# Optimization experiments

Hardware: AMD Instinct MI355X
Metric: run time of the kernel (lower is better)

Reference implementation:

```python
import jax, jax.numpy as jnp
import numpy as np

HEADS, DEPTH, KS = 4, 16, 3
PAD = KS // 2
LN_EPS = 1e-3   # keras LayerNormalization default
BN_EPS = 1e-3   # keras BatchNormalization default


def _layernorm(x, g, b):
    m = jnp.mean(x, axis=-1, keepdims=True)
    v = jnp.var(x, axis=-1, keepdims=True)
    return (x - m) * jax.lax.rsqrt(v + LN_EPS) * g + b


def setup_inputs() -> dict:
    key = jax.random.key(0)
    ks = jax.random.split(key, 12)
    B, H, W, C, FF = 4, 384, 384, 64, 128
    s = 0.05
    return {
        "x": jax.random.normal(ks[0], (B, H, W, C), jnp.float32),
        "wq": jax.random.normal(ks[1], (C, C), jnp.float32) * s,
        "wk": jax.random.normal(ks[2], (C, C), jnp.float32) * s,
        "wv": jax.random.normal(ks[3], (C, C), jnp.float32) * s,
        "ln1_g": jnp.ones((C,), jnp.float32),
        "ln1_b": jnp.zeros((C,), jnp.float32),
        "ff1_w": jax.random.normal(ks[4], (C, FF), jnp.float32) * s,
        "ff1_b": jnp.zeros((FF,), jnp.float32),
        "ff2_w": jax.random.normal(ks[5], (FF, C), jnp.float32) * s,
        "ff2_b": jnp.zeros((C,), jnp.float32),
        "ln2_g": jnp.ones((C,), jnp.float32),
        "ln2_b": jnp.zeros((C,), jnp.float32),
        "w_fuse": jax.random.normal(ks[6], (C, C), jnp.float32) * s,
        "bn_g": jax.random.uniform(ks[7], (C,), jnp.float32, 0.5, 1.5),
        "bn_b": jax.random.normal(ks[8], (C,), jnp.float32) * s,
        "bn_mean": jax.random.normal(ks[9], (C,), jnp.float32) * s,
        "bn_var": jax.random.uniform(ks[10], (C,), jnp.float32, 0.5, 1.5),
    }


def reference(x, wq, wk, wv, ln1_g, ln1_b, ff1_w, ff1_b, ff2_w, ff2_b,
              ln2_g, ln2_b, w_fuse, bn_g, bn_b, bn_mean, bn_var):
    B, H, W, C = x.shape
    # 1x1-conv projections == per-pixel dense over channels
    q = jnp.einsum('bhwc,cd->bhwd', x, wq).reshape(B, H, W, HEADS, DEPTH)
    k = jnp.einsum('bhwc,cd->bhwd', x, wk)
    v = jnp.einsum('bhwc,cd->bhwd', x, wv)
    # SAME zero-padding, matching tf.image.extract_patches
    kp = jnp.pad(k, ((0, 0), (PAD, PAD), (PAD, PAD), (0, 0)))
    vp = jnp.pad(v, ((0, 0), (PAD, PAD), (PAD, PAD), (0, 0)))
    # scores for each of the ks*ks offsets via shifted slices (no im2col blowup)
    sims = []
    for dy in range(KS):
        for dx in range(KS):
            ksh = kp[:, dy:dy + H, dx:dx + W, :].reshape(B, H, W, HEADS, DEPTH)
            sims.append(jnp.einsum('bhwnd,bhwnd->bhwn', q, ksh))
    sim = jnp.stack(sims, axis=3) / jnp.sqrt(jnp.float32(DEPTH))  # [B,H,W,ka,heads]
    attn = jax.nn.softmax(sim, axis=3)
    out = jnp.zeros_like(q)  # [B,H,W,heads,depth]
    i = 0
    for dy in range(KS):
        for dx in range(KS):
            vsh = vp[:, dy:dy + H, dx:dx + W, :].reshape(B, H, W, HEADS, DEPTH)
            out = out + attn[:, :, :, i, :, None] * vsh
            i += 1
    out = out.reshape(B, H, W, C)
    # residual (res_proj is None since C % heads == 0) + LN
    out = _layernorm(x + out, ln1_g, ln1_b)
    # token FFN with residual + LN
    ff = jax.nn.relu(jnp.einsum('bhwc,cf->bhwf', out, ff1_w) + ff1_b)
    ff = jnp.einsum('bhwf,fc->bhwc', ff, ff2_w) + ff2_b
    out = _layernorm(out + ff, ln2_g, ln2_b)
    # fuse 1x1 conv + BN (inference mode, moving stats) + relu
    out = jnp.einsum('bhwc,cd->bhwd', out, w_fuse)
    scale = bn_g * jax.lax.rsqrt(bn_var + BN_EPS)
    out = out * scale + (bn_b - bn_mean * scale)
    return jax.nn.relu(out)
```

## Files before the change

kernel.cpp:

```cpp
#include <hip/hip_runtime.h>

#define MTOT 589824

typedef __attribute__((ext_vector_type(8))) short bf16x8;
typedef __attribute__((ext_vector_type(4))) float f32x4;
#define MFMA16 __builtin_amdgcn_mfma_f32_16x16x32_bf16

__device__ __forceinline__ unsigned short f2bf(float f) {
    union { float f; unsigned u; } x; x.f = f;
    unsigned r = x.u + 0x7FFFu + ((x.u >> 16) & 1u);
    return (unsigned short)(r >> 16);
}
__device__ __forceinline__ float bf2f(unsigned short h) {
    union { unsigned u; float f; } x; x.u = ((unsigned)h) << 16;
    return x.f;
}
__device__ __forceinline__ float2 bfpair(int v) {
    union { unsigned u; float f; } a, b;
    a.u = ((unsigned)v) << 16;
    b.u = ((unsigned)v) & 0xffff0000u;
    return make_float2(a.f, b.f);
}
__device__ __forceinline__ int is_bf16(const void* ln1g) {
    return ((const unsigned short*)ln1g)[0] != 0;
}
__device__ __forceinline__ float ldp(const void* p, int i, int isbf) {
    return isbf ? bf2f(((const unsigned short*)p)[i]) : ((const float*)p)[i];
}

__global__ void k_prep(const void* wq, const void* wk, const void* wv,
                       const void* ln1g, const void* ln1b,
                       const void* ff1w, const void* ff1b,
                       const void* ff2w, const void* ff2b,
                       const void* ln2g, const void* ln2b,
                       const void* wfuse, const void* bng, const void* bnb,
                       const void* bnm, const void* bnv,
                       unsigned short* Wbase, float* P) {
    const int isbf = is_bf16(ln1g);
    const int tid = blockIdx.x * blockDim.x + threadIdx.x;
    const int stride = gridDim.x * blockDim.x;
    unsigned short* Wqkv = Wbase;
    unsigned short* W1 = Wbase + 12288;
    unsigned short* W2 = W1 + 8192;
    unsigned short* WF = W2 + 8192;
    for (int i = tid; i < 12288; i += stride) {
        int n = i >> 6, k = i & 63;
        float v;
        if (n < 64)        v = ldp(wq, k*64 + n, isbf) * 0.25f;
        else if (n < 128)  v = ldp(wk, k*64 + (n-64), isbf);
        else               v = ldp(wv, k*64 + (n-128), isbf);
        Wqkv[n*64 + k] = f2bf(v);
    }
    for (int i = tid; i < 8192; i += stride) {
        int n = i >> 6, k = i & 63;
        W1[n*64 + k] = f2bf(ldp(ff1w, k*128 + n, isbf));
    }
    for (int i = tid; i < 8192; i += stride) {
        int n = i >> 7, k = i & 127;
        W2[n*128 + k] = f2bf(ldp(ff2w, k*64 + n, isbf));
    }
    for (int i = tid; i < 4096; i += stride) {
        int n = i >> 6, k = i & 63;
        WF[n*64 + k] = f2bf(ldp(wfuse, k*64 + n, isbf));
    }
    for (int i = tid; i < 64; i += stride) {
        P[i]       = ldp(ln1g, i, isbf);
        P[64+i]    = ldp(ln1b, i, isbf);
        P[256+i]   = ldp(ff2b, i, isbf);
        P[320+i]   = ldp(ln2g, i, isbf);
        P[384+i]   = ldp(ln2b, i, isbf);
        float sc   = ldp(bng, i, isbf) * rsqrtf(ldp(bnv, i, isbf) + 1e-3f);
        P[448+i]   = sc;
        P[512+i]   = ldp(bnb, i, isbf) - ldp(bnm, i, isbf) * sc;
    }
    for (int i = tid; i < 128; i += stride) P[128+i] = ldp(ff1b, i, isbf);
}

__global__ __launch_bounds__(256) void k_qkv(const void* __restrict__ xg,
                                             const void* __restrict__ ln1g,
                                             const unsigned short* __restrict__ Wqkv,
                                             unsigned short* __restrict__ qp,
                                             unsigned short* __restrict__ kvp) {
    __shared__ unsigned short lA[64*72];
    __shared__ unsigned short stg[64*200];
    const int t = threadIdx.x;
    const long m0 = (long)blockIdx.x * 64;
    if (is_bf16(ln1g)) {
        const unsigned short* xs = (const unsigned short*)xg + m0*64;
        #pragma unroll
        for (int j = 0; j < 2; ++j) {
            int e = (j*256 + t)*8, r = e >> 6, c = e & 63;
            *(int4*)&lA[r*72 + c] = *(const int4*)(xs + e);
        }
    } else {
        const float* xs = (const float*)xg + m0*64;
        #pragma unroll
        for (int j = 0; j < 4; ++j) {
            int e = (j*256 + t)*4, r = e >> 6, c = e & 63;
            float4 f = *(const float4*)(xs + e);
            ushort4 h;
            h.x = f2bf(f.x); h.y = f2bf(f.y); h.z = f2bf(f.z); h.w = f2bf(f.w);
            *(ushort4*)&lA[r*72 + c] = h;
        }
    }
    __syncthreads();
    const int w = t >> 6, l = t & 63, lm = l & 15, q4 = l >> 4;
    const bf16x8 a0 = *(const bf16x8*)&lA[(w*16 + lm)*72 + q4*8];
    const bf16x8 a1 = *(const bf16x8*)&lA[(w*16 + lm)*72 + 32 + q4*8];
    #pragma unroll
    for (int nt = 0; nt < 12; ++nt) {
        const unsigned short* wp = Wqkv + (nt*16 + lm)*64 + q4*8;
        bf16x8 b0 = *(const bf16x8*)wp;
        bf16x8 b1 = *(const bf16x8*)(wp + 32);
        f32x4 acc = {0.f, 0.f, 0.f, 0.f};
        acc = MFMA16(a0, b0, acc, 0, 0, 0);
        acc = MFMA16(a1, b1, acc, 0, 0, 0);
        #pragma unroll
        for (int r = 0; r < 4; ++r)
            stg[(w*16 + q4*4 + r)*200 + nt*16 + lm] = f2bf(acc[r]);
    }
    __syncthreads();
    const size_t P16 = (size_t)MTOT * 16, P32 = (size_t)MTOT * 32;
    #pragma unroll
    for (int j = 0; j < 2; ++j) {
        int idx = j*256 + t;
        int h = idx >> 7, rem = idx & 127, px = rem >> 1, part = rem & 1;
        *(int4*)(qp + (size_t)h*P16 + (m0 + px)*16 + part*8) =
            *(const int4*)&stg[px*200 + h*16 + part*8];
    }
    #pragma unroll
    for (int j = 0; j < 4; ++j) {
        int idx = j*256 + t;
        int h = idx >> 8, rem = idx & 255, px = rem >> 2, part = rem & 3;
        int scol = (part < 2) ? (64 + h*16 + part*8) : (128 + h*16 + (part-2)*8);
        *(int4*)(kvp + (size_t)h*P32 + (m0 + px)*32 + part*8) =
            *(const int4*)&stg[px*200 + scol];
    }
}

__global__ __launch_bounds__(256) void k_attn(unsigned short* __restrict__ qp,
                                              const unsigned short* __restrict__ kvp) {
    __shared__ unsigned short kvh[324*36];
    const int t = threadIdx.x;
    const int h = blockIdx.x & 3;
    const int tile = blockIdx.x >> 2;
    const int bx = tile % 24;
    const int by = (tile / 24) % 24;
    const int bb = tile / 576;
    const long imgbase = (long)bb * 384 * 384;
    const unsigned short* kvplane = kvp + (size_t)h * MTOT * 32;
    unsigned short* qplane = qp + (size_t)h * MTOT * 16;

    for (int i = t; i < 2592; i += 256) {
        int p = i >> 3, part = i & 7;
        int hy = p / 18, hx = p - hy*18;
        int gy = by*16 + hy - 1, gx = bx*16 + hx - 1;
        int2 val = {0, 0};
        if (gy >= 0 && gy < 384 && gx >= 0 && gx < 384)
            val = *(const int2*)(kvplane + (imgbase + (long)gy*384 + gx)*32 + part*4);
        *(int2*)&kvh[p*36 + part*4] = val;
    }
    __syncthreads();

    const int tx = t & 15, ty = t >> 4;
    const long pix = imgbase + (long)(by*16 + ty)*384 + bx*16 + tx;
    float qv[16];
    {
        const int4 qa = *(const int4*)(qplane + pix*16);
        const int4 qb = *(const int4*)(qplane + pix*16 + 8);
        float2 p0;
        p0 = bfpair(qa.x); qv[0]  = p0.x; qv[1]  = p0.y;
        p0 = bfpair(qa.y); qv[2]  = p0.x; qv[3]  = p0.y;
        p0 = bfpair(qa.z); qv[4]  = p0.x; qv[5]  = p0.y;
        p0 = bfpair(qa.w); qv[6]  = p0.x; qv[7]  = p0.y;
        p0 = bfpair(qb.x); qv[8]  = p0.x; qv[9]  = p0.y;
        p0 = bfpair(qb.y); qv[10] = p0.x; qv[11] = p0.y;
        p0 = bfpair(qb.z); qv[12] = p0.x; qv[13] = p0.y;
        p0 = bfpair(qb.w); qv[14] = p0.x; qv[15] = p0.y;
    }
    float w9[9];
    #pragma unroll
    for (int e = 0; e < 9; ++e) {
        int dy = e / 3, dx = e - dy*3;
        const int2* kp = (const int2*)&kvh[((ty+dy)*18 + tx+dx)*36];
        float sacc = 0.f;
        #pragma unroll
        for (int j = 0; j < 4; ++j) {
            int2 kk = kp[j];
            float2 pa = bfpair(kk.x), pb = bfpair(kk.y);
            sacc += qv[j*4+0]*pa.x + qv[j*4+1]*pa.y
                  + qv[j*4+2]*pb.x + qv[j*4+3]*pb.y;
        }
        w9[e] = sacc;
    }
    float mx = w9[0];
    #pragma unroll
    for (int e = 1; e < 9; ++e) mx = fmaxf(mx, w9[e]);
    float den = 0.f;
    #pragma unroll
    for (int e = 0; e < 9; ++e) { w9[e] = __expf(w9[e] - mx); den += w9[e]; }
    const float inv = 1.f / den;
    float att[16];
    #pragma unroll
    for (int i = 0; i < 16; ++i) att[i] = 0.f;
    #pragma unroll
    for (int e = 0; e < 9; ++e) {
        int dy = e / 3, dx = e - dy*3;
        const int2* vp = (const int2*)&kvh[((ty+dy)*18 + tx+dx)*36 + 16];
        const float wgt = w9[e] * inv;
        #pragma unroll
        for (int j = 0; j < 4; ++j) {
            int2 vv = vp[j];
            float2 pa = bfpair(vv.x), pb = bfpair(vv.y);
            att[j*4+0] += wgt*pa.x;
            att[j*4+1] += wgt*pa.y;
            att[j*4+2] += wgt*pb.x;
            att[j*4+3] += wgt*pb.y;
        }
    }
    int4 o0, o1;
    o0.x = (int)((unsigned)f2bf(att[0])  | ((unsigned)f2bf(att[1])  << 16));
    o0.y = (int)((unsigned)f2bf(att[2])  | ((unsigned)f2bf(att[3])  << 16));
    o0.z = (int)((unsigned)f2bf(att[4])  | ((unsigned)f2bf(att[5])  << 16));
    o0.w = (int)((unsigned)f2bf(att[6])  | ((unsigned)f2bf(att[7])  << 16));
    o1.x = (int)((unsigned)f2bf(att[8])  | ((unsigned)f2bf(att[9])  << 16));
    o1.y = (int)((unsigned)f2bf(att[10]) | ((unsigned)f2bf(att[11]) << 16));
    o1.z = (int)((unsigned)f2bf(att[12]) | ((unsigned)f2bf(att[13]) << 16));
    o1.w = (int)((unsigned)f2bf(att[14]) | ((unsigned)f2bf(att[15]) << 16));
    *(int4*)(qplane + pix*16)     = o0;
    *(int4*)(qplane + pix*16 + 8) = o1;
}

__global__ __launch_bounds__(256) void k_tail(const unsigned short* __restrict__ attp,
                                              const void* __restrict__ xg,
                                              const void* __restrict__ ln1g,
                                              const unsigned short* __restrict__ W1,
                                              const unsigned short* __restrict__ W2,
                                              const unsigned short* __restrict__ WF,
                                              const float* __restrict__ P,
                                              void* __restrict__ outg) {
    __shared__ unsigned short lA[64*72];
    __shared__ unsigned short hbuf[64*136];
    const int t = threadIdx.x;
    const long m0 = (long)blockIdx.x * 64;
    const int isbf = is_bf16(ln1g);
    const size_t P16 = (size_t)MTOT * 16;
    #pragma unroll
    for (int j = 0; j < 2; ++j) {
        int idx = j*256 + t;
        int h = idx >> 7, rem = idx & 127, px = rem >> 1, part = rem & 1;
        *(int4*)&lA[px*72 + h*16 + part*8] =
            *(const int4*)(attp + (size_t)h*P16 + (m0 + px)*16 + part*8);
    }
    __syncthreads();
    {
        const int px = t >> 2, qtr = t & 3;
        float v[16];
        const int2* ap = (const int2*)&lA[px*72 + qtr*16];
        #pragma unroll
        for (int j = 0; j < 4; ++j) {
            int2 u = ap[j];
            float2 pa = bfpair(u.x), pb = bfpair(u.y);
            v[j*4+0] = pa.x; v[j*4+1] = pa.y; v[j*4+2] = pb.x; v[j*4+3] = pb.y;
        }
        if (isbf) {
            const int4* xp = (const int4*)((const unsigned short*)xg + (m0 + px)*64 + qtr*16);
            #pragma unroll
            for (int j = 0; j < 2; ++j) {
                int4 u = xp[j];
                float2 pa = bfpair(u.x), pb = bfpair(u.y), pc = bfpair(u.z), pd = bfpair(u.w);
                v[j*8+0] += pa.x; v[j*8+1] += pa.y;
                v[j*8+2] += pb.x; v[j*8+3] += pb.y;
                v[j*8+4] += pc.x; v[j*8+5] += pc.y;
                v[j*8+6] += pd.x; v[j*8+7] += pd.y;
            }
        } else {
            const float4* xp = (const float4*)((const float*)xg + (m0 + px)*64 + qtr*16);
            #pragma unroll
            for (int j = 0; j < 4; ++j) {
                float4 f = xp[j];
                v[j*4+0] += f.x; v[j*4+1] += f.y; v[j*4+2] += f.z; v[j*4+3] += f.w;
            }
        }
        float s = 0.f, ss = 0.f;
        #pragma unroll
        for (int c = 0; c < 16; ++c) { s += v[c]; ss += v[c]*v[c]; }
        s  += __shfl_xor(s, 1);  ss += __shfl_xor(ss, 1);
        s  += __shfl_xor(s, 2);  ss += __shfl_xor(ss, 2);
        const float mean = s * (1.f/64.f);
        const float var  = ss * (1.f/64.f) - mean*mean;
        const float rs   = rsqrtf(var + 1e-3f);
        unsigned short* wp = &lA[px*72 + qtr*16];
        #pragma unroll
        for (int c = 0; c < 16; ++c)
            wp[c] = f2bf((v[c] - mean)*rs*P[qtr*16 + c] + P[64 + qtr*16 + c]);
    }
    __syncthreads();
    const int w = t >> 6, l = t & 63, lm = l & 15, q4 = l >> 4;
    {
        const bf16x8 a0 = *(const bf16x8*)&lA[(w*16 + lm)*72 + q4*8];
        const bf16x8 a1 = *(const bf16x8*)&lA[(w*16 + lm)*72 + 32 + q4*8];
        #pragma unroll
        for (int nt = 0; nt < 8; ++nt) {
            const unsigned short* wp = W1 + (nt*16 + lm)*64 + q4*8;
            bf16x8 b0 = *(const bf16x8*)wp;
            bf16x8 b1 = *(const bf16x8*)(wp + 32);
            f32x4 acc = {0.f, 0.f, 0.f, 0.f};
            acc = MFMA16(a0, b0, acc, 0, 0, 0);
            acc = MFMA16(a1, b1, acc, 0, 0, 0);
            const float bias = P[128 + nt*16 + lm];
            #pragma unroll
            for (int r = 0; r < 4; ++r)
                hbuf[(w*16 + q4*4 + r)*136 + nt*16 + lm] = f2bf(fmaxf(acc[r] + bias, 0.f));
        }
    }
    __syncthreads();
    {
        bf16x8 a[4];
        #pragma unroll
        for (int kc = 0; kc < 4; ++kc)
            a[kc] = *(const bf16x8*)&hbuf[(w*16 + lm)*136 + kc*32 + q4*8];
        float v[4][4];
        #pragma unroll
        for (int nt = 0; nt < 4; ++nt) {
            f32x4 acc = {0.f, 0.f, 0.f, 0.f};
            #pragma unroll
            for (int kc = 0; kc < 4; ++kc) {
                bf16x8 b = *(const bf16x8*)(W2 + (nt*16 + lm)*128 + kc*32 + q4*8);
                acc = MFMA16(a[kc], b, acc, 0, 0, 0);
            }
            const int col = nt*16 + lm;
            const float bias = P[256 + col];
            #pragma unroll
            for (int r = 0; r < 4; ++r)
                v[nt][r] = acc[r] + bias + bf2f(lA[(w*16 + q4*4 + r)*72 + col]);
        }
        float s[4], ss[4];
        #pragma unroll
        for (int r = 0; r < 4; ++r) {
            s[r]  = v[0][r] + v[1][r] + v[2][r] + v[3][r];
            ss[r] = v[0][r]*v[0][r] + v[1][r]*v[1][r] + v[2][r]*v[2][r] + v[3][r]*v[3][r];
        }
        #pragma unroll
        for (int mk = 1; mk <= 8; mk <<= 1) {
            #pragma unroll
            for (int r = 0; r < 4; ++r) {
                s[r]  += __shfl_xor(s[r], mk);
                ss[r] += __shfl_xor(ss[r], mk);
            }
        }
        __syncthreads();
        #pragma unroll
        for (int r = 0; r < 4; ++r) {
            const float mean = s[r] * (1.f/64.f);
            const float var  = ss[r] * (1.f/64.f) - mean*mean;
            const float rsv  = rsqrtf(var + 1e-3f);
            #pragma unroll
            for (int nt = 0; nt < 4; ++nt) {
                const int col = nt*16 + lm;
                lA[(w*16 + q4*4 + r)*72 + col] =
                    f2bf((v[nt][r] - mean)*rsv*P[320 + col] + P[384 + col]);
            }
        }
    }
    __syncthreads();
    {
        const bf16x8 a0 = *(const bf16x8*)&lA[(w*16 + lm)*72 + q4*8];
        const bf16x8 a1 = *(const bf16x8*)&lA[(w*16 + lm)*72 + 32 + q4*8];
        float* stf = (float*)hbuf + w*1024;
        unsigned short* sth = hbuf + w*1024;
        #pragma unroll
        for (int nt = 0; nt < 4; ++nt) {
            const unsigned short* wp = WF + (nt*16 + lm)*64 + q4*8;
            bf16x8 b0 = *(const bf16x8*)wp;
            bf16x8 b1 = *(const bf16x8*)(wp + 32);
            f32x4 acc = {0.f, 0.f, 0.f, 0.f};
            acc = MFMA16(a0, b0, acc, 0, 0, 0);
            acc = MFMA16(a1, b1, acc, 0, 0, 0);
            const int col = nt*16 + lm;
            const float sc = P[448 + col], bi = P[512 + col];
            #pragma unroll
            for (int r = 0; r < 4; ++r) {
                float f = fmaxf(acc[r]*sc + bi, 0.f);
                if (isbf) sth[(q4*4 + r)*64 + col] = f2bf(f);
                else      stf[(q4*4 + r)*64 + col] = f;
            }
        }
    }
    __syncthreads();
    if (isbf) {
        const unsigned short* sth = hbuf + w*1024;
        unsigned short* orow = (unsigned short*)outg + m0*64;
        #pragma unroll
        for (int i = 0; i < 2; ++i) {
            int e = (i*64 + l)*8, r = e >> 6, c = e & 63;
            *(int4*)(orow + (long)(w*16 + r)*64 + c) = *(const int4*)&sth[e];
        }
    } else {
        const float* stf = (const float*)hbuf + w*1024;
        float* orow = (float*)outg + m0*64;
        #pragma unroll
        for (int i = 0; i < 4; ++i) {
            int e = (i*64 + l)*4, r = e >> 6, c = e & 63;
            *(float4*)(orow + (long)(w*16 + r)*64 + c) = *(const float4*)&stf[e];
        }
    }
}

extern "C" void kernel_launch(void* const* d_in, const int* in_sizes, int n_in,
                              void* d_out, int out_size, void* d_ws, size_t ws_size,
                              hipStream_t stream) {
    const void* x     = d_in[0];
    const void* wq    = d_in[1];
    const void* wk    = d_in[2];
    const void* wv    = d_in[3];
    const void* ln1g  = d_in[4];
    const void* ln1b  = d_in[5];
    const void* ff1w  = d_in[6];
    const void* ff1b  = d_in[7];
    const void* ff2w  = d_in[8];
    const void* ff2b  = d_in[9];
    const void* ln2g  = d_in[10];
    const void* ln2b  = d_in[11];
    const void* wfuse = d_in[12];
    const void* bng   = d_in[13];
    const void* bnb   = d_in[14];
    const void* bnm   = d_in[15];
    const void* bnv   = d_in[16];

    unsigned short* qp  = (unsigned short*)d_ws;
    unsigned short* kvp = qp + (size_t)4 * MTOT * 16;
    unsigned short* Wbase = kvp + (size_t)4 * MTOT * 32;
    float* P = (float*)(Wbase + 32768);

    k_prep<<<64, 256, 0, stream>>>(wq, wk, wv, ln1g, ln1b, ff1w, ff1b, ff2w, ff2b,
                                   ln2g, ln2b, wfuse, bng, bnb, bnm, bnv, Wbase, P);
    k_qkv <<<MTOT/64, 256, 0, stream>>>(x, ln1g, Wbase, qp, kvp);
    k_attn<<<9216,    256, 0, stream>>>(qp, kvp);
    k_tail<<<MTOT/64, 256, 0, stream>>>(qp, x, ln1g,
                                        Wbase + 12288, Wbase + 20480, Wbase + 28672,
                                        P, d_out);
}
```

Baseline: 621.1 us.

## Fuse QKV projection, local attention and FFN tail into one tiled kernel

Replaces the three kernels (QKV projection, 3x3 neighbourhood attention, FFN/LN/fuse tail) with a single kernel working on 8x8 pixel tiles. Each tile loads a 10x10 halo of x into swizzled LDS and recomputes K/V for the halo pixels in place. This removes the global round trip of the q/k/v intermediates, about 113 MB of bf16 writes plus reads. In exchange the K/V projection is redone for halo pixels (100 rows instead of 64), LDS use per block grows, and block indices are remapped with a stride across image regions.

```diff
diff --git a/kernel.cpp b/kernel.cpp
--- a/kernel.cpp
+++ b/kernel.cpp
@@ -76,40 +76,86 @@
     for (int i = tid; i < 128; i += stride) P[128+i] = ldp(ff1b, i, isbf);
 }
 
-__global__ __launch_bounds__(256) void k_qkv(const void* __restrict__ xg,
-                                             const void* __restrict__ ln1g,
-                                             const unsigned short* __restrict__ Wqkv,
-                                             unsigned short* __restrict__ qp,
-                                             unsigned short* __restrict__ kvp) {
-    __shared__ unsigned short lA[64*72];
-    __shared__ unsigned short stg[64*200];
+__device__ __forceinline__ int rowOf(int hy, int hx) {
+    if (hy >= 1 && hy <= 8 && hx >= 1 && hx <= 8) return (hy - 1) * 8 + (hx - 1);
+    if (hy == 0) return 64 + hx;
+    if (hy == 9) return 74 + hx;
+    if (hx == 0) return 84 + (hy - 1);
+    return 92 + (hy - 1);
+}
+
+__global__ __launch_bounds__(256) void k_fused(
+    const void* __restrict__ xg, const void* __restrict__ ln1g,
+    const unsigned short* __restrict__ Wqkv, const unsigned short* __restrict__ W1,
+    const unsigned short* __restrict__ W2, const unsigned short* __restrict__ WF,
+    const float* __restrict__ P, void* __restrict__ outg) {
+    __shared__ __align__(16) unsigned short xh[112 * 64];
+    __shared__ __align__(16) unsigned short kvb[112 * 132];
+    __shared__ __align__(16) unsigned short qy[64 * 72];
     const int t = threadIdx.x;
-    const long m0 = (long)blockIdx.x * 64;
-    if (is_bf16(ln1g)) {
-        const unsigned short* xs = (const unsigned short*)xg + m0*64;
-        #pragma unroll
-        for (int j = 0; j < 2; ++j) {
-            int e = (j*256 + t)*8, r = e >> 6, c = e & 63;
-            *(int4*)&lA[r*72 + c] = *(const int4*)(xs + e);
+    const int isbf = is_bf16(ln1g);
+    const int bid = ((int)blockIdx.x & 7) * 1152 + ((int)blockIdx.x >> 3);
+    const int bb = bid / 2304;
+    const int tile = bid - bb * 2304;
+    const int by = tile / 48, bx = tile - by * 48;
+    const long imgbase = (long)bb * 147456;
+
+    if (isbf) {
+        const unsigned short* xs = (const unsigned short*)xg;
+        for (int i = t; i < 800; i += 256) {
+            int p = i >> 3, c8 = i & 7;
+            int hy = p / 10, hx = p - hy * 10;
+            int r = rowOf(hy, hx);
+            int gy = by * 8 + hy - 1, gx = bx * 8 + hx - 1;
+            int4 val = {0, 0, 0, 0};
+            if ((unsigned)gy < 384u && (unsigned)gx < 384u)
+                val = *(const int4*)(xs + (imgbase + (long)gy * 384 + gx) * 64 + c8 * 8);
+            *(int4*)&xh[r * 64 + ((c8 ^ (r & 7)) << 3)] = val;
         }
     } else {
-        const float* xs = (const float*)xg + m0*64;
-        #pragma unroll
-        for (int j = 0; j < 4; ++j) {
-            int e = (j*256 + t)*4, r = e >> 6, c = e & 63;
-            float4 f = *(const float4*)(xs + e);
-            ushort4 h;
-            h.x = f2bf(f.x); h.y = f2bf(f.y); h.z = f2bf(f.z); h.w = f2bf(f.w);
-            *(ushort4*)&lA[r*72 + c] = h;
-        }
-    }
-    __syncthreads();
+        const float* xs = (const float*)xg;
+        for (int i = t; i < 1600; i += 256) {
+            int p = i >> 4, c4 = i & 15;
+            int hy = p / 10, hx = p - hy * 10;
+            int r = rowOf(hy, hx);
+            int gy = by * 8 + hy - 1, gx = bx * 8 + hx - 1;
+            ushort4 hv = {0, 0, 0, 0};
+            if ((unsigned)gy < 384u && (unsigned)gx < 384u) {
+                float4 f = *(const float4*)(xs + (imgbase + (long)gy * 384 + gx) * 64 + c4 * 4);
+                hv.x = f2bf(f.x); hv.y = f2bf(f.y); hv.z = f2bf(f.z); hv.w = f2bf(f.w);
+            }
+            int c8 = c4 >> 1;
+            *(ushort4*)&xh[r * 64 + (((c8 ^ (r & 7)) << 3) | ((c4 & 1) << 2))] = hv;
+        }
+    }
+    if (t < 96) {
+        int4 zz = {0, 0, 0, 0};
+        *(int4*)&xh[(100 + (t >> 3)) * 64 + ((t & 7) << 3)] = zz;
+    }
+
+    float4 rf0, rf1, rf2, rf3; int4 ri0, ri1;
+    {
+        const int px = t >> 2, qtr = t & 3;
+        const long pofs = (imgbase + (long)(by*8 + (px >> 3)) * 384 + bx*8 + (px & 7)) * 64 + qtr * 16;
+        if (isbf) {
+            const int4* xp = (const int4*)((const unsigned short*)xg + pofs);
+            ri0 = xp[0]; ri1 = xp[1];
+        } else {
+            const float4* xp = (const float4*)((const float*)xg + pofs);
+            rf0 = xp[0]; rf1 = xp[1]; rf2 = xp[2]; rf3 = xp[3];
+        }
+    }
+    __syncthreads();
+
     const int w = t >> 6, l = t & 63, lm = l & 15, q4 = l >> 4;
-    const bf16x8 a0 = *(const bf16x8*)&lA[(w*16 + lm)*72 + q4*8];
-    const bf16x8 a1 = *(const bf16x8*)&lA[(w*16 + lm)*72 + 32 + q4*8];
-    #pragma unroll
-    for (int nt = 0; nt < 12; ++nt) {
-        const unsigned short* wp = Wqkv + (nt*16 + lm)*64 + q4*8;
+    #pragma unroll 2
+    for (int uu = 0; uu < 14; ++uu) {
+        int u = uu * 4 + w;
+        int rt = u >> 3, nt = u & 7;
+        int row = rt * 16 + lm, sw = row & 7;
+        const bf16x8 a0 = *(const bf16x8*)&xh[row * 64 + ((q4 ^ sw) << 3)];
+        const bf16x8 a1 = *(const bf16x8*)&xh[row * 64 + (((q4 + 4) ^ sw) << 3)];
+        const unsigned short* wp = Wqkv + (64 + nt * 16 + lm) * 64 + q4 * 8;
         bf16x8 b0 = *(const bf16x8*)wp;
         bf16x8 b1 = *(const bf16x8*)(wp + 32);
         f32x4 acc = {0.f, 0.f, 0.f, 0.f};
@@ -117,146 +163,103 @@
         acc = MFMA16(a1, b1, acc, 0, 0, 0);
         #pragma unroll
         for (int r = 0; r < 4; ++r)
-            stg[(w*16 + q4*4 + r)*200 + nt*16 + lm] = f2bf(acc[r]);
-    }
-    __syncthreads();
-    const size_t P16 = (size_t)MTOT * 16, P32 = (size_t)MTOT * 32;
+            kvb[(rt * 16 + q4 * 4 + r) * 132 + nt * 16 + lm] = f2bf(acc[r]);
+    }
     #pragma unroll
-    for (int j = 0; j < 2; ++j) {
-        int idx = j*256 + t;
-        int h = idx >> 7, rem = idx & 127, px = rem >> 1, part = rem & 1;
-        *(int4*)(qp + (size_t)h*P16 + (m0 + px)*16 + part*8) =
-            *(const int4*)&stg[px*200 + h*16 + part*8];
-    }
-    #pragma unroll
-    for (int j = 0; j < 4; ++j) {
-        int idx = j*256 + t;
-        int h = idx >> 8, rem = idx & 255, px = rem >> 2, part = rem & 3;
-        int scol = (part < 2) ? (64 + h*16 + part*8) : (128 + h*16 + (part-2)*8);
-        *(int4*)(kvp + (size_t)h*P32 + (m0 + px)*32 + part*8) =
-            *(const int4*)&stg[px*200 + scol];
-    }
-}
-
-__global__ __launch_bounds__(256) void k_attn(unsigned short* __restrict__ qp,
-                                              const unsigned short* __restrict__ kvp) {
-    __shared__ unsigned short kvh[324*36];
-    const int t = threadIdx.x;
-    const int h = blockIdx.x & 3;
-    const int tile = blockIdx.x >> 2;
-    const int bx = tile % 24;
-    const int by = (tile / 24) % 24;
-    const int bb = tile / 576;
-    const long imgbase = (long)bb * 384 * 384;
-    const unsigned short* kvplane = kvp + (size_t)h * MTOT * 32;
-    unsigned short* qplane = qp + (size_t)h * MTOT * 16;
-
-    for (int i = t; i < 2592; i += 256) {
-        int p = i >> 3, part = i & 7;
-        int hy = p / 18, hx = p - hy*18;
-        int gy = by*16 + hy - 1, gx = bx*16 + hx - 1;
-        int2 val = {0, 0};
-        if (gy >= 0 && gy < 384 && gx >= 0 && gx < 384)
-            val = *(const int2*)(kvplane + (imgbase + (long)gy*384 + gx)*32 + part*4);
-        *(int2*)&kvh[p*36 + part*4] = val;
-    }
-    __syncthreads();
-
-    const int tx = t & 15, ty = t >> 4;
-    const long pix = imgbase + (long)(by*16 + ty)*384 + bx*16 + tx;
-    float qv[16];
-    {
-        const int4 qa = *(const int4*)(qplane + pix*16);
-        const int4 qb = *(const int4*)(qplane + pix*16 + 8);
-        float2 p0;
-        p0 = bfpair(qa.x); qv[0]  = p0.x; qv[1]  = p0.y;
-        p0 = bfpair(qa.y); qv[2]  = p0.x; qv[3]  = p0.y;
-        p0 = bfpair(qa.z); qv[4]  = p0.x; qv[5]  = p0.y;
-        p0 = bfpair(qa.w); qv[6]  = p0.x; qv[7]  = p0.y;
-        p0 = bfpair(qb.x); qv[8]  = p0.x; qv[9]  = p0.y;
-        p0 = bfpair(qb.y); qv[10] = p0.x; qv[11] = p0.y;
-        p0 = bfpair(qb.z); qv[12] = p0.x; qv[13] = p0.y;
-        p0 = bfpair(qb.w); qv[14] = p0.x; qv[15] = p0.y;
-    }
-    float w9[9];
-    #pragma unroll
-    for (int e = 0; e < 9; ++e) {
-        int dy = e / 3, dx = e - dy*3;
-        const int2* kp = (const int2*)&kvh[((ty+dy)*18 + tx+dx)*36];
-        float sacc = 0.f;
-        #pragma unroll
-        for (int j = 0; j < 4; ++j) {
-            int2 kk = kp[j];
-            float2 pa = bfpair(kk.x), pb = bfpair(kk.y);
-            sacc += qv[j*4+0]*pa.x + qv[j*4+1]*pa.y
-                  + qv[j*4+2]*pb.x + qv[j*4+3]*pb.y;
-        }
-        w9[e] = sacc;
-    }
-    float mx = w9[0];
-    #pragma unroll
-    for (int e = 1; e < 9; ++e) mx = fmaxf(mx, w9[e]);
-    float den = 0.f;
-    #pragma unroll
-    for (int e = 0; e < 9; ++e) { w9[e] = __expf(w9[e] - mx); den += w9[e]; }
-    const float inv = 1.f / den;
-    float att[16];
-    #pragma unroll
-    for (int i = 0; i < 16; ++i) att[i] = 0.f;
-    #pragma unroll
-    for (int e = 0; e < 9; ++e) {
-        int dy = e / 3, dx = e - dy*3;
-        const int2* vp = (const int2*)&kvh[((ty+dy)*18 + tx+dx)*36 + 16];
-        const float wgt = w9[e] * inv;
-        #pragma unroll
-        for (int j = 0; j < 4; ++j) {
-            int2 vv = vp[j];
-            float2 pa = bfpair(vv.x), pb = bfpair(vv.y);
-            att[j*4+0] += wgt*pa.x;
-            att[j*4+1] += wgt*pa.y;
-            att[j*4+2] += wgt*pb.x;
-            att[j*4+3] += wgt*pb.y;
-        }
-    }
-    int4 o0, o1;
-    o0.x = (int)((unsigned)f2bf(att[0])  | ((unsigned)f2bf(att[1])  << 16));
-    o0.y = (int)((unsigned)f2bf(att[2])  | ((unsigned)f2bf(att[3])  << 16));
-    o0.z = (int)((unsigned)f2bf(att[4])  | ((unsigned)f2bf(att[5])  << 16));
-    o0.w = (int)((unsigned)f2bf(att[6])  | ((unsigned)f2bf(att[7])  << 16));
-    o1.x = (int)((unsigned)f2bf(att[8])  | ((unsigned)f2bf(att[9])  << 16));
-    o1.y = (int)((unsigned)f2bf(att[10]) | ((unsigned)f2bf(att[11]) << 16));
-    o1.z = (int)((unsigned)f2bf(att[12]) | ((unsigned)f2bf(att[13]) << 16));
-    o1.w = (int)((unsigned)f2bf(att[14]) | ((unsigned)f2bf(att[15]) << 16));
-    *(int4*)(qplane + pix*16)     = o0;
-    *(int4*)(qplane + pix*16 + 8) = o1;
-}
-
-__global__ __launch_bounds__(256) void k_tail(const unsigned short* __restrict__ attp,
-                                              const void* __restrict__ xg,
-                                              const void* __restrict__ ln1g,
-                                              const unsigned short* __restrict__ W1,
-                                              const unsigned short* __restrict__ W2,
-                                              const unsigned short* __restrict__ WF,
-                                              const float* __restrict__ P,
-                                              void* __restrict__ outg) {
-    __shared__ unsigned short lA[64*72];
-    __shared__ unsigned short hbuf[64*136];
-    const int t = threadIdx.x;
-    const long m0 = (long)blockIdx.x * 64;
-    const int isbf = is_bf16(ln1g);
-    const size_t P16 = (size_t)MTOT * 16;
-    #pragma unroll
-    for (int j = 0; j < 2; ++j) {
-        int idx = j*256 + t;
-        int h = idx >> 7, rem = idx & 127, px = rem >> 1, part = rem & 1;
-        *(int4*)&lA[px*72 + h*16 + part*8] =
-            *(const int4*)(attp + (size_t)h*P16 + (m0 + px)*16 + part*8);
-    }
-    __syncthreads();
+    for (int uu = 0; uu < 4; ++uu) {
+        int row = uu * 16 + lm, sw = row & 7;
+        const bf16x8 a0 = *(const bf16x8*)&xh[row * 64 + ((q4 ^ sw) << 3)];
+        const bf16x8 a1 = *(const bf16x8*)&xh[row * 64 + (((q4 + 4) ^ sw) << 3)];
+        const unsigned short* wp = Wqkv + (w * 16 + lm) * 64 + q4 * 8;
+        bf16x8 b0 = *(const bf16x8*)wp;
+        bf16x8 b1 = *(const bf16x8*)(wp + 32);
+        f32x4 acc = {0.f, 0.f, 0.f, 0.f};
+        acc = MFMA16(a0, b0, acc, 0, 0, 0);
+        acc = MFMA16(a1, b1, acc, 0, 0, 0);
+        #pragma unroll
+        for (int r = 0; r < 4; ++r)
+            qy[(uu * 16 + q4 * 4 + r) * 72 + w * 16 + lm] = f2bf(acc[r]);
+    }
+    __syncthreads();
+
+    {
+        const int h = w, py = l >> 3, px8 = l & 7;
+        float qv[16];
+        {
+            const int4* qp2 = (const int4*)&qy[l * 72 + h * 16];
+            int4 qa = qp2[0], qb4 = qp2[1];
+            float2 p0;
+            p0 = bfpair(qa.x);  qv[0]  = p0.x; qv[1]  = p0.y;
+            p0 = bfpair(qa.y);  qv[2]  = p0.x; qv[3]  = p0.y;
+            p0 = bfpair(qa.z);  qv[4]  = p0.x; qv[5]  = p0.y;
+            p0 = bfpair(qa.w);  qv[6]  = p0.x; qv[7]  = p0.y;
+            p0 = bfpair(qb4.x); qv[8]  = p0.x; qv[9]  = p0.y;
+            p0 = bfpair(qb4.y); qv[10] = p0.x; qv[11] = p0.y;
+            p0 = bfpair(qb4.z); qv[12] = p0.x; qv[13] = p0.y;
+            p0 = bfpair(qb4.w); qv[14] = p0.x; qv[15] = p0.y;
+        }
+        int rn9[9];
+        #pragma unroll
+        for (int e = 0; e < 9; ++e) {
+            int dy = e / 3, dx = e - dy * 3;
+            rn9[e] = rowOf(py + dy, px8 + dx);
+        }
+        float w9[9];
+        #pragma unroll
+        for (int e = 0; e < 9; ++e) {
+            const int2* kp = (const int2*)&kvb[rn9[e] * 132 + h * 16];
+            float sacc = 0.f;
+            #pragma unroll
+            for (int j = 0; j < 4; ++j) {
+                int2 kk = kp[j];
+                float2 pa = bfpair(kk.x), pb = bfpair(kk.y);
+                sacc += qv[j*4+0]*pa.x + qv[j*4+1]*pa.y
+                      + qv[j*4+2]*pb.x + qv[j*4+3]*pb.y;
+            }
+            w9[e] = sacc;
+        }
+        float mx = w9[0];
+        #pragma unroll
+        for (int e = 1; e < 9; ++e) mx = fmaxf(mx, w9[e]);
+        float den = 0.f;
+        #pragma unroll
+        for (int e = 0; e < 9; ++e) { w9[e] = __expf(w9[e] - mx); den += w9[e]; }
+        const float inv = 1.f / den;
+        float att[16];
+        #pragma unroll
+        for (int i = 0; i < 16; ++i) att[i] = 0.f;
+        #pragma unroll
+        for (int e = 0; e < 9; ++e) {
+            const int2* vp = (const int2*)&kvb[rn9[e] * 132 + 64 + h * 16];
+            const float wgt = w9[e] * inv;
+            #pragma unroll
+            for (int j = 0; j < 4; ++j) {
+                int2 vv = vp[j];
+                float2 pa = bfpair(vv.x), pb = bfpair(vv.y);
+                att[j*4+0] += wgt*pa.x;
+                att[j*4+1] += wgt*pa.y;
+                att[j*4+2] += wgt*pb.x;
+                att[j*4+3] += wgt*pb.y;
+            }
+        }
+        int4 o0, o1;
+        o0.x = (int)((unsigned)f2bf(att[0])  | ((unsigned)f2bf(att[1])  << 16));
+        o0.y = (int)((unsigned)f2bf(att[2])  | ((unsigned)f2bf(att[3])  << 16));
+        o0.z = (int)((unsigned)f2bf(att[4])  | ((unsigned)f2bf(att[5])  << 16));
+        o0.w = (int)((unsigned)f2bf(att[6])  | ((unsigned)f2bf(att[7])  << 16));
+        o1.x = (int)((unsigned)f2bf(att[8])  | ((unsigned)f2bf(att[9])  << 16));
+        o1.y = (int)((unsigned)f2bf(att[10]) | ((unsigned)f2bf(att[11]) << 16));
+        o1.z = (int)((unsigned)f2bf(att[12]) | ((unsigned)f2bf(att[13]) << 16));
+        o1.w = (int)((unsigned)f2bf(att[14]) | ((unsigned)f2bf(att[15]) << 16));
+        *(int4*)&qy[l * 72 + h * 16]     = o0;
+        *(int4*)&qy[l * 72 + h * 16 + 8] = o1;
+    }
+    __syncthreads();
+
     {
         const int px = t >> 2, qtr = t & 3;
         float v[16];
-        const int2* ap = (const int2*)&lA[px*72 + qtr*16];
+        const int2* ap = (const int2*)&qy[px * 72 + qtr * 16];
         #pragma unroll
         for (int j = 0; j < 4; ++j) {
             int2 u = ap[j];
@@ -264,23 +267,17 @@
             v[j*4+0] = pa.x; v[j*4+1] = pa.y; v[j*4+2] = pb.x; v[j*4+3] = pb.y;
         }
         if (isbf) {
-            const int4* xp = (const int4*)((const unsigned short*)xg + (m0 + px)*64 + qtr*16);
-            #pragma unroll
-            for (int j = 0; j < 2; ++j) {
-                int4 u = xp[j];
-                float2 pa = bfpair(u.x), pb = bfpair(u.y), pc = bfpair(u.z), pd = bfpair(u.w);
-                v[j*8+0] += pa.x; v[j*8+1] += pa.y;
-                v[j*8+2] += pb.x; v[j*8+3] += pb.y;
-                v[j*8+4] += pc.x; v[j*8+5] += pc.y;
-                v[j*8+6] += pd.x; v[j*8+7] += pd.y;
-            }
+            float2 pa = bfpair(ri0.x), pb = bfpair(ri0.y), pc = bfpair(ri0.z), pd = bfpair(ri0.w);
+            v[0] += pa.x; v[1] += pa.y; v[2] += pb.x; v[3] += pb.y;
+            v[4] += pc.x; v[5] += pc.y; v[6] += pd.x; v[7] += pd.y;
+            pa = bfpair(ri1.x); pb = bfpair(ri1.y); pc = bfpair(ri1.z); pd = bfpair(ri1.w);
+            v[8]  += pa.x; v[9]  += pa.y; v[10] += pb.x; v[11] += pb.y;
+            v[12] += pc.x; v[13] += pc.y; v[14] += pd.x; v[15] += pd.y;
         } else {
-            const float4* xp = (const float4*)((const float*)xg + (m0 + px)*64 + qtr*16);
-            #pragma unroll
-            for (int j = 0; j < 4; ++j) {
-                float4 f = xp[j];
-                v[j*4+0] += f.x; v[j*4+1] += f.y; v[j*4+2] += f.z; v[j*4+3] += f.w;
-            }
+            v[0]  += rf0.x; v[1]  += rf0.y; v[2]  += rf0.z; v[3]  += rf0.w;
+            v[4]  += rf1.x; v[5]  += rf1.y; v[6]  += rf1.z; v[7]  += rf1.w;
+            v[8]  += rf2.x; v[9]  += rf2.y; v[10] += rf2.z; v[11] += rf2.w;
+            v[12] += rf3.x; v[13] += rf3.y; v[14] += rf3.z; v[15] += rf3.w;
         }
         float s = 0.f, ss = 0.f;
         #pragma unroll
@@ -290,16 +287,17 @@
         const float mean = s * (1.f/64.f);
         const float var  = ss * (1.f/64.f) - mean*mean;
         const float rs   = rsqrtf(var + 1e-3f);
-        unsigned short* wp = &lA[px*72 + qtr*16];
+        unsigned short* wp2 = &qy[px * 72 + qtr * 16];
         #pragma unroll
         for (int c = 0; c < 16; ++c)
-            wp[c] = f2bf((v[c] - mean)*rs*P[qtr*16 + c] + P[64 + qtr*16 + c]);
-    }
-    __syncthreads();
-    const int w = t >> 6, l = t & 63, lm = l & 15, q4 = l >> 4;
-    {
-        const bf16x8 a0 = *(const bf16x8*)&lA[(w*16 + lm)*72 + q4*8];
-        const bf16x8 a1 = *(const bf16x8*)&lA[(w*16 + lm)*72 + 32 + q4*8];
+            wp2[c] = f2bf((v[c] - mean)*rs*P[qtr*16 + c] + P[64 + qtr*16 + c]);
+    }
+    __syncthreads();
+
+    unsigned short* hh = kvb;
+    {
+        const bf16x8 a0 = *(const bf16x8*)&qy[(w*16 + lm)*72 + q4*8];
+        const bf16x8 a1 = *(const bf16x8*)&qy[(w*16 + lm)*72 + 32 + q4*8];
         #pragma unroll
         for (int nt = 0; nt < 8; ++nt) {
             const unsigned short* wp = W1 + (nt*16 + lm)*64 + q4*8;
@@ -311,7 +309,7 @@
             const float bias = P[128 + nt*16 + lm];
             #pragma unroll
             for (int r = 0; r < 4; ++r)
-                hbuf[(w*16 + q4*4 + r)*136 + nt*16 + lm] = f2bf(fmaxf(acc[r] + bias, 0.f));
+                hh[(w*16 + q4*4 + r)*136 + nt*16 + lm] = f2bf(fmaxf(acc[r] + bias, 0.f));
         }
     }
     __syncthreads();
@@ -319,8 +317,8 @@
         bf16x8 a[4];
         #pragma unroll
         for (int kc = 0; kc < 4; ++kc)
-            a[kc] = *(const bf16x8*)&hbuf[(w*16 + lm)*136 + kc*32 + q4*8];
-        float v[4][4];
+            a[kc] = *(const bf16x8*)&hh[(w*16 + lm)*136 + kc*32 + q4*8];
+        float v2[4][4];
         #pragma unroll
         for (int nt = 0; nt < 4; ++nt) {
             f32x4 acc = {0.f, 0.f, 0.f, 0.f};
@@ -333,13 +331,13 @@
             const float bias = P[256 + col];
             #pragma unroll
             for (int r = 0; r < 4; ++r)
-                v[nt][r] = acc[r] + bias + bf2f(lA[(w*16 + q4*4 + r)*72 + col]);
+                v2[nt][r] = acc[r] + bias + bf2f(qy[(w*16 + q4*4 + r)*72 + col]);
         }
         float s[4], ss[4];
         #pragma unroll
         for (int r = 0; r < 4; ++r) {
-            s[r]  = v[0][r] + v[1][r] + v[2][r] + v[3][r];
-            ss[r] = v[0][r]*v[0][r] + v[1][r]*v[1][r] + v[2][r]*v[2][r] + v[3][r]*v[3][r];
+            s[r]  = v2[0][r] + v2[1][r] + v2[2][r] + v2[3][r];
+            ss[r] = v2[0][r]*v2[0][r] + v2[1][r]*v2[1][r] + v2[2][r]*v2[2][r] + v2[3][r]*v2[3][r];
         }
         #pragma unroll
         for (int mk = 1; mk <= 8; mk <<= 1) {
@@ -358,17 +356,17 @@
             #pragma unroll
             for (int nt = 0; nt < 4; ++nt) {
                 const int col = nt*16 + lm;
-                lA[(w*16 + q4*4 + r)*72 + col] =
-                    f2bf((v[nt][r] - mean)*rsv*P[320 + col] + P[384 + col]);
-            }
-        }
-    }
-    __syncthreads();
-    {
-        const bf16x8 a0 = *(const bf16x8*)&lA[(w*16 + lm)*72 + q4*8];
-        const bf16x8 a1 = *(const bf16x8*)&lA[(w*16 + lm)*72 + 32 + q4*8];
-        float* stf = (float*)hbuf + w*1024;
-        unsigned short* sth = hbuf + w*1024;
+                qy[(w*16 + q4*4 + r)*72 + col] =
+                    f2bf((v2[nt][r] - mean)*rsv*P[320 + col] + P[384 + col]);
+            }
+        }
+    }
+    __syncthreads();
+    {
+        const bf16x8 a0 = *(const bf16x8*)&qy[(w*16 + lm)*72 + q4*8];
+        const bf16x8 a1 = *(const bf16x8*)&qy[(w*16 + lm)*72 + 32 + q4*8];
+        float* stf = (float*)kvb + w*1024;
+        unsigned short* sth = kvb + w*1024;
         #pragma unroll
         for (int nt = 0; nt < 4; ++nt) {
             const unsigned short* wp = WF + (nt*16 + lm)*64 + q4*8;
@@ -389,20 +387,24 @@
     }
     __syncthreads();
     if (isbf) {
-        const unsigned short* sth = hbuf + w*1024;
-        unsigned short* orow = (unsigned short*)outg + m0*64;
+        const unsigned short* sth = kvb + w*1024;
+        unsigned short* op = (unsigned short*)outg;
         #pragma unroll
         for (int i = 0; i < 2; ++i) {
             int e = (i*64 + l)*8, r = e >> 6, c = e & 63;
-            *(int4*)(orow + (long)(w*16 + r)*64 + c) = *(const int4*)&sth[e];
+            int px = w*16 + r;
+            long ga = (imgbase + (long)(by*8 + (px >> 3))*384 + bx*8 + (px & 7))*64 + c;
+            *(int4*)(op + ga) = *(const int4*)&sth[e];
         }
     } else {
-        const float* stf = (const float*)hbuf + w*1024;
-        float* orow = (float*)outg + m0*64;
+        const float* stf = (const float*)kvb + w*1024;
+        float* op = (float*)outg;
         #pragma unroll
         for (int i = 0; i < 4; ++i) {
             int e = (i*64 + l)*4, r = e >> 6, c = e & 63;
-            *(float4*)(orow + (long)(w*16 + r)*64 + c) = *(const float4*)&stf[e];
+            int px = w*16 + r;
+            long ga = (imgbase + (long)(by*8 + (px >> 3))*384 + bx*8 + (px & 7))*64 + c;
+            *(float4*)(op + ga) = *(const float4*)&stf[e];
         }
     }
 }
@@ -428,16 +430,11 @@
     const void* bnm   = d_in[15];
     const void* bnv   = d_in[16];
 
-    unsigned short* qp  = (unsigned short*)d_ws;
-    unsigned short* kvp = qp + (size_t)4 * MTOT * 16;
-    unsigned short* Wbase = kvp + (size_t)4 * MTOT * 32;
+    unsigned short* Wbase = (unsigned short*)d_ws;
     float* P = (float*)(Wbase + 32768);
 
     k_prep<<<64, 256, 0, stream>>>(wq, wk, wv, ln1g, ln1b, ff1w, ff1b, ff2w, ff2b,
                                    ln2g, ln2b, wfuse, bng, bnb, bnm, bnv, Wbase, P);
-    k_qkv <<<MTOT/64, 256, 0, stream>>>(x, ln1g, Wbase, qp, kvp);
-    k_attn<<<9216,    256, 0, stream>>>(qp, kvp);
-    k_tail<<<MTOT/64, 256, 0, stream>>>(qp, x, ln1g,
-                                        Wbase + 12288, Wbase + 20480, Wbase + 28672,
-                                        P, d_out);
-}
+    k_fused<<<9216, 256, 0, stream>>>(x, ln1g, Wbase, Wbase + 12288, Wbase + 20480,
+                                      Wbase + 28672, P, d_out);
+}
```

Result: faster. 603.0 us (-2.9%).
